# Optimization experiments

Measured on AMD Instinct MI355X. Metric: run time of the kernel, lower is better.

Reference implementation:

```python
import jax, jax.numpy as jnp
import numpy as np

DIM = 768
NUM_HEADS = 12
WIN = (32, 32)  # pretrain window == runtime (H, W)


def _build_rel_pos_idx(wh, ww):
    coords = np.stack(np.meshgrid(np.arange(wh), np.arange(ww), indexing='ij'))  # (2,wh,ww)
    flat = coords.reshape(2, -1)  # (2, N)
    rel = flat[:, :, None] - flat[:, None, :]  # (2, N, N)
    rel = rel.transpose(1, 2, 0).astype(np.int64)  # (N, N, 2)
    rel[:, :, 0] += wh - 1
    rel[:, :, 1] += ww - 1
    rel[:, :, 0] *= 2 * ww - 1
    return rel.sum(-1)  # (N, N) in [0, (2wh-1)(2ww-1))


def setup_inputs() -> dict:
    key = jax.random.key(0)
    ks = jax.random.split(key, 7)
    wh, ww = WIN
    num_rel = (2 * wh - 1) * (2 * ww - 1) + 3  # 3972
    x = jax.random.normal(ks[0], (8, wh, ww, DIM), dtype=jnp.float32)
    qkv_w = jax.random.normal(ks[1], (3 * DIM, DIM), dtype=jnp.float32) * 0.02
    q_bias = jnp.zeros((DIM,), dtype=jnp.float32)
    v_bias = jnp.zeros((DIM,), dtype=jnp.float32)
    rel_bias_table = jax.random.normal(ks[2], (num_rel, NUM_HEADS), dtype=jnp.float32) * 0.02
    proj_w = jax.random.normal(ks[3], (DIM, DIM), dtype=jnp.float32) * 0.02
    proj_b = jnp.zeros((DIM,), dtype=jnp.float32)
    rel_pos_idx = jnp.asarray(_build_rel_pos_idx(wh, ww), dtype=jnp.int32)  # (N, N)
    return {"x": x, "qkv_w": qkv_w, "q_bias": q_bias, "v_bias": v_bias,
            "rel_bias_table": rel_bias_table, "proj_w": proj_w, "proj_b": proj_b,
            "rel_pos_idx": rel_pos_idx}


def reference(x, qkv_w, q_bias, v_bias, rel_bias_table, proj_w, proj_b, rel_pos_idx):
    B, H, W, C = x.shape
    nH = rel_bias_table.shape[-1]
    hd = C // nH
    N = H * W
    scale = hd ** -0.5
    # qkv with (q_bias, 0, v_bias) bias layout as in BEiT
    qkv_bias = jnp.concatenate([q_bias, jnp.zeros_like(v_bias), v_bias])
    qkv = x.reshape(B, N, C) @ qkv_w.T + qkv_bias  # (B, N, 3C)
    qkv = qkv.reshape(B, N, 3, nH, hd).transpose(2, 0, 3, 1, 4)  # (3, B, nH, N, hd)
    q, k, v = qkv[0], qkv[1], qkv[2]
    attn = jnp.einsum('bhnd,bhmd->bhnm', q * scale, k)  # (B, nH, N, N)
    # gathered relative-position bias: table[(N,N)] -> (N, N, nH) -> (nH, N, N)
    bias = rel_bias_table[rel_pos_idx].transpose(2, 0, 1)
    attn = jax.nn.softmax(attn + bias[None], axis=-1)
    out = jnp.einsum('bhnm,bhmd->bhnd', attn, v)  # (B, nH, N, hd)
    out = out.transpose(0, 2, 1, 3).reshape(B, H, W, C)
    return out @ proj_w.T + proj_b
```

## Files before the change

kernel.cpp:

```cpp
#include <hip/hip_runtime.h>
#include <stdint.h>

using u16 = unsigned short;
using u32 = unsigned int;

typedef __bf16 bf16x8 __attribute__((ext_vector_type(8)));
typedef float f32x4 __attribute__((ext_vector_type(4)));

__device__ __forceinline__ u16 f2bf(float f){
  u32 u = __float_as_uint(f);
  return (u16)((u + 0x7FFFu + ((u >> 16) & 1u)) >> 16);
}
__device__ __forceinline__ float bf2f(u16 h){
  return __uint_as_float(((u32)h) << 16);
}
__device__ __forceinline__ void split2(float x, u16& hi, u16& lo){
  hi = f2bf(x);
  lo = f2bf(x - bf2f(hi));
}
template<int SH>
__device__ __forceinline__ int swz(int off){ return off ^ (((off >> SH) & 7) << 4); }

__device__ __forceinline__ void gload16(const u16* g, u16* l){
  __builtin_amdgcn_global_load_lds(
      (const __attribute__((address_space(1))) void*)g,
      (__attribute__((address_space(3))) void*)l, 16, 0, 0);
}

__global__ __launch_bounds__(256) void k_split(const float* __restrict__ src,
                                               u16* __restrict__ hi,
                                               u16* __restrict__ lo)
{
  int i = blockIdx.x * 256 + threadIdx.x;
  float4 v = ((const float4*)src)[i];
  ushort4 h, l;
  split2(v.x, h.x, l.x);
  split2(v.y, h.y, l.y);
  split2(v.z, h.z, l.z);
  split2(v.w, h.w, l.w);
  ((ushort4*)hi)[i] = h;
  ((ushort4*)lo)[i] = l;
}

__global__ __launch_bounds__(256) void k_bias(const int* __restrict__ relidx,
                                              const float* __restrict__ table,
                                              u16* __restrict__ bias)
{
  int q = blockIdx.x;
  int j0 = threadIdx.x * 4;
  int4 idx = *(const int4*)(relidx + q * 1024 + j0);
#pragma unroll
  for (int h = 0; h < 12; ++h){
    ushort4 o;
    o.x = f2bf(table[(size_t)idx.x * 12 + h]);
    o.y = f2bf(table[(size_t)idx.y * 12 + h]);
    o.z = f2bf(table[(size_t)idx.z * 12 + h]);
    o.w = f2bf(table[(size_t)idx.w * 12 + h]);
    *(ushort4*)(bias + ((size_t)h << 20) + q * 1024 + j0) = o;
  }
}

__global__ __launch_bounds__(512) void k_g256(
    const u16* __restrict__ A0, const u16* __restrict__ A1, const u16* __restrict__ A2,
    const u16* __restrict__ B0, const u16* __restrict__ B1, const u16* __restrict__ B2,
    const float* __restrict__ bq, const float* __restrict__ bv,
    u16* __restrict__ QKhi, u16* __restrict__ QKlo,
    u16* __restrict__ Vthi, u16* __restrict__ Vtlo)
{
  extern __shared__ u16 R[];
  const int tid = threadIdx.x;
  const int lane = tid & 63;
  const int wid = tid >> 6;
  const int wm = wid >> 2, wn = wid & 3;
  const int g = lane >> 4, cl = lane & 15;
  const int orig = blockIdx.y * gridDim.x + blockIdx.x;
  const int cpx = (gridDim.x * gridDim.y) >> 3;
  const int wg = (orig & 7) * cpx + (orig >> 3);
  const int bx = wg % gridDim.x, by = wg / gridDim.x;
  const int bm = by << 8, bn = bx << 8;
  const int rlane = lane >> 2;
  const int csrc = (lane & 3) ^ ((lane >> 3) & 3);

  f32x4 acc[8][4];
  f32x4 z4 = {0.f, 0.f, 0.f, 0.f};
#pragma unroll
  for (int i = 0; i < 8; ++i)
#pragma unroll
    for (int j = 0; j < 4; ++j) acc[i][j] = z4;

  auto stageA = [&](int t){
    int tt = (t < 72) ? t : t - 72;
    int ph = (tt >= 48) ? 2 : ((tt >= 24) ? 1 : 0);
    int kin = (tt - ph * 24) * 32;
    const u16* Ap = ph == 0 ? A0 : (ph == 1 ? A1 : A2);
    const int sb = (t & 3) * 16384;
#pragma unroll
    for (int i = 0; i < 2; ++i){
      int rA = (wid * 2 + i) * 16 + rlane;
      gload16(Ap + (size_t)(bm + rA) * 768 + kin + csrc * 8,
              &R[sb + (wid * 2 + i) * 512]);
    }
  };
  auto stageB = [&](int t){
    int tt = (t < 72) ? t : t - 72;
    int ph = (tt >= 48) ? 2 : ((tt >= 24) ? 1 : 0);
    int kin = (tt - ph * 24) * 32;
    const u16* Bp = ph == 0 ? B0 : (ph == 1 ? B1 : B2);
    const int sb = (t & 3) * 16384 + 8192;
#pragma unroll
    for (int i = 0; i < 2; ++i){
      int rB = (wid * 2 + i) * 16 + rlane;
      gload16(Bp + (size_t)(bn + rB) * 768 + kin + csrc * 8,
              &R[sb + (wid * 2 + i) * 512]);
    }
  };
  auto rf = [&](const u16* base, int row) -> bf16x8 {
    return *(const bf16x8*)(base + row * 32 + ((g ^ ((cl >> 1) & 3)) << 3));
  };

  stageA(0); stageB(0); stageA(1); stageB(1); stageA(2); stageB(2);

  for (int t = 0; t < 72; ++t){
    asm volatile("s_waitcnt vmcnt(8)" ::: "memory");
    __builtin_amdgcn_s_barrier();
    __builtin_amdgcn_sched_barrier(0);
    const u16* Ab = &R[(t & 3) * 16384];
    const u16* Bb = Ab + 8192;
    stageA(t + 3);
    bf16x8 bfv[4], af[4];
#pragma unroll
    for (int nf = 0; nf < 4; ++nf) bfv[nf] = rf(Bb, wn * 64 + nf * 16 + cl);
#pragma unroll
    for (int mf = 0; mf < 4; ++mf) af[mf] = rf(Ab, wm * 128 + mf * 16 + cl);
    asm volatile("s_waitcnt lgkmcnt(0)" ::: "memory");
    __builtin_amdgcn_sched_barrier(0);
    __builtin_amdgcn_s_setprio(1);
#pragma unroll
    for (int mf = 0; mf < 4; ++mf)
#pragma unroll
      for (int nf = 0; nf < 4; ++nf)
        acc[mf][nf] = __builtin_amdgcn_mfma_f32_16x16x32_bf16(af[mf], bfv[nf], acc[mf][nf], 0, 0, 0);
    __builtin_amdgcn_s_setprio(0);
    __builtin_amdgcn_s_barrier();
    __builtin_amdgcn_sched_barrier(0);
    stageB(t + 3);
#pragma unroll
    for (int mf = 0; mf < 4; ++mf) af[mf] = rf(Ab, wm * 128 + (mf + 4) * 16 + cl);
    asm volatile("s_waitcnt lgkmcnt(0)" ::: "memory");
    __builtin_amdgcn_sched_barrier(0);
    __builtin_amdgcn_s_setprio(1);
#pragma unroll
    for (int mf = 0; mf < 4; ++mf)
#pragma unroll
      for (int nf = 0; nf < 4; ++nf)
        acc[mf + 4][nf] = __builtin_amdgcn_mfma_f32_16x16x32_bf16(af[mf], bfv[nf], acc[mf + 4][nf], 0, 0, 0);
    __builtin_amdgcn_s_setprio(0);
  }

  const int bb = bm >> 10;
  const int tokb = bm & 1023;
  u16* Hs = R;
  u16* Ls = R + 8192;

  if (bx < 6){
    const bool isQ = (bx < 3);
#pragma unroll
    for (int c = 0; c < 8; ++c){
      __syncthreads();
      if (wm == (c >> 2)){
#pragma unroll
        for (int mi = 0; mi < 2; ++mi){
          const int mf = (c & 3) * 2 + mi;
#pragma unroll
          for (int nf = 0; nf < 4; ++nf){
            int col = wn * 64 + nf * 16 + cl;
            float bqv = isQ ? bq[bn + col] : 0.f;
#pragma unroll
            for (int r = 0; r < 4; ++r){
              float v = acc[mf][nf][r];
              if (isQ) v = (v + bqv) * 0.125f;
              u16 hi, lo; split2(v, hi, lo);
              int idx = (mi * 16 + g * 4 + r) * 256 + col;
              Hs[idx] = hi;
              Ls[idx] = lo;
            }
          }
        }
      }
      __syncthreads();
#pragma unroll
      for (int i = 0; i < 2; ++i){
        int s = tid + i * 512;
        int rr = s >> 5, seg = s & 31;
        size_t gb = (size_t)(bm + c * 32 + rr) * 1536 + bn + seg * 8;
        *(float4*)(QKhi + gb) = *(const float4*)(Hs + rr * 256 + seg * 8);
        *(float4*)(QKlo + gb) = *(const float4*)(Ls + rr * 256 + seg * 8);
      }
    }
  } else {
    const int ccolbase = bn - 1536;
#pragma unroll
    for (int c = 0; c < 8; ++c){
      __syncthreads();
      if (wn == (c >> 1)){
#pragma unroll
        for (int nf2 = 0; nf2 < 2; ++nf2){
          const int nf = (c & 1) * 2 + nf2;
          int cc = nf2 * 16 + cl;
          float bvv = bv[ccolbase + c * 32 + cc];
#pragma unroll
          for (int mf = 0; mf < 8; ++mf){
            ushort4 h4, l4;
            u16 hh_, ll_;
            split2(acc[mf][nf][0] + bvv, hh_, ll_); h4.x = hh_; l4.x = ll_;
            split2(acc[mf][nf][1] + bvv, hh_, ll_); h4.y = hh_; l4.y = ll_;
            split2(acc[mf][nf][2] + bvv, hh_, ll_); h4.z = hh_; l4.z = ll_;
            split2(acc[mf][nf][3] + bvv, hh_, ll_); h4.w = hh_; l4.w = ll_;
            int m0 = wm * 128 + mf * 16 + g * 4;
            int off = cc * 512 + m0 * 2;
            *(ushort4*)((char*)Hs + swz<9>(off)) = h4;
            *(ushort4*)((char*)Ls + swz<9>(off)) = l4;
          }
        }
      }
      __syncthreads();
#pragma unroll
      for (int i = 0; i < 2; ++i){
        int s = tid + i * 512;
        int drr = s >> 5, seg = s & 31;
        int off = drr * 512 + seg * 16;
        int ccol = ccolbase + c * 32 + drr;
        int hh = ccol >> 6, d = ccol & 63;
        size_t gb = ((size_t)(bb * 12 + hh) * 64 + d) * 1024 + tokb + seg * 8;
        *(float4*)(Vthi + gb) = *(const float4*)((char*)Hs + swz<9>(off));
        *(float4*)(Vtlo + gb) = *(const float4*)((char*)Ls + swz<9>(off));
      }
    }
  }
}

__global__ __launch_bounds__(256) void k_proj(
    const u16* __restrict__ A0, const u16* __restrict__ A1, const u16* __restrict__ A2,
    const u16* __restrict__ B0, const u16* __restrict__ B1, const u16* __restrict__ B2,
    const float* __restrict__ pb,
    float* __restrict__ Cout)
{
  __shared__ __align__(16) u16 As[4][128 * 32];
  __shared__ __align__(16) u16 Bs[4][128 * 32];
  const int tid = threadIdx.x;
  const int lane = tid & 63;
  const int wid = tid >> 6;
  const int wr = wid >> 1, wc = wid & 1;
  const int g = lane >> 4, cl = lane & 15;
  const int orig = blockIdx.y * gridDim.x + blockIdx.x;
  const int cpx = (gridDim.x * gridDim.y) >> 3;
  const int wg = (orig & 7) * cpx + (orig >> 3);
  const int bx = wg % gridDim.x, by = wg / gridDim.x;
  const int bm = by << 7, bn = bx << 7;
  const int srow = lane >> 2;
  const int sseg = ((lane & 3) ^ ((lane >> 3) & 3)) * 8;
  const int gph  = (g ^ ((cl >> 1) & 3)) * 8;

  f32x4 acc[4][4];
  f32x4 z4 = {0.f, 0.f, 0.f, 0.f};
#pragma unroll
  for (int i = 0; i < 4; ++i)
#pragma unroll
    for (int j = 0; j < 4; ++j) acc[i][j] = z4;

  auto stage = [&](int t){
    int tt = (t < 72) ? t : t - 72;
    int ph = (tt >= 48) ? 2 : ((tt >= 24) ? 1 : 0);
    int kin = (tt - ph * 24) * 32;
    const u16* Ap = ph == 0 ? A0 : (ph == 1 ? A1 : A2);
    const u16* Bp = ph == 0 ? B0 : (ph == 1 ? B1 : B2);
    const int slot = t & 3;
#pragma unroll
    for (int c = 0; c < 2; ++c){
      int chunk = wid * 2 + c;
      int row = chunk * 16 + srow;
      gload16(Ap + (size_t)(bm + row) * 768 + kin + sseg, &As[slot][chunk * 512]);
      gload16(Bp + (size_t)(bn + row) * 768 + kin + sseg, &Bs[slot][chunk * 512]);
    }
  };

  stage(0); stage(1); stage(2);
  for (int t = 0; t < 72; ++t){
    asm volatile("s_waitcnt vmcnt(8)" ::: "memory");
    __builtin_amdgcn_s_barrier();
    __builtin_amdgcn_sched_barrier(0);
    stage(t + 3);
    const int slot = t & 3;
    bf16x8 af[4], bfv[4];
#pragma unroll
    for (int mf = 0; mf < 4; ++mf)
      af[mf] = *(const bf16x8*)(&As[slot][(wr * 64 + mf * 16 + cl) * 32 + gph]);
#pragma unroll
    for (int nf = 0; nf < 4; ++nf)
      bfv[nf] = *(const bf16x8*)(&Bs[slot][(wc * 64 + nf * 16 + cl) * 32 + gph]);
    asm volatile("s_waitcnt lgkmcnt(0)" ::: "memory");
    __builtin_amdgcn_sched_barrier(0);
    __builtin_amdgcn_s_setprio(1);
#pragma unroll
    for (int mf = 0; mf < 4; ++mf)
#pragma unroll
      for (int nf = 0; nf < 4; ++nf)
        acc[mf][nf] = __builtin_amdgcn_mfma_f32_16x16x32_bf16(af[mf], bfv[nf], acc[mf][nf], 0, 0, 0);
    __builtin_amdgcn_s_setprio(0);
  }

  __syncthreads();
#pragma unroll
  for (int mf = 0; mf < 4; ++mf)
#pragma unroll
    for (int nf = 0; nf < 4; ++nf)
#pragma unroll
      for (int r = 0; r < 4; ++r){
        int m = bm + wr * 64 + mf * 16 + g * 4 + r;
        int n = bn + wc * 64 + nf * 16 + cl;
        Cout[(size_t)m * 768 + n] = acc[mf][nf][r] + pb[n];
      }
}

__global__ __launch_bounds__(256) void k_attn(
    const u16* __restrict__ QKhi, const u16* __restrict__ QKlo,
    const u16* __restrict__ Vthi, const u16* __restrict__ Vtlo,
    const u16* __restrict__ bias,
    u16* __restrict__ Ohi, u16* __restrict__ Olo)
{
  __shared__ __align__(16) u16 lds[36864];
  const int KH0 = 0, KL0 = 8192, VH0 = 16384, VL0 = 24576, PS = 32768;

  const int tid = threadIdx.x;
  const int lane = tid & 63;
  const int w = tid >> 6;
  const int g = lane >> 4, cl = lane & 15;
  const int qt = blockIdx.x;
  const int b  = blockIdx.y;
  const int h  = blockIdx.z;
  const size_t rowbase = (size_t)b * 1024;
  const size_t bhv = (size_t)(b * 12 + h) * (1024 * 64);
  const u16* bias_w = bias + ((size_t)h << 20) + (size_t)(qt * 64 + w * 16) * 1024;

  const int dr = lane >> 3, dc = lane & 7;
  const int csrc = dc ^ dr;
  const size_t kbase = (rowbase + w * 16 + dr) * 1536 + 768 + (size_t)h * 64 + csrc * 8;
  const size_t vbase = bhv + (size_t)(w * 16 + dr) * 1024 + csrc * 8;

  auto stage = [&](int buf, int jt){
#pragma unroll
    for (int i = 0; i < 2; ++i){
      int r0 = (w * 16 + i * 8) * 64;
      size_t ko = kbase + (size_t)(jt * 64 + i * 8) * 1536;
      size_t vo = vbase + (size_t)i * 8 * 1024 + jt * 64;
      gload16(QKhi + ko, &lds[KH0 + buf * 4096 + r0]);
      gload16(QKlo + ko, &lds[KL0 + buf * 4096 + r0]);
      gload16(Vthi + vo, &lds[VH0 + buf * 4096 + r0]);
      gload16(Vtlo + vo, &lds[VL0 + buf * 4096 + r0]);
    }
  };
  auto tread = [&](int base, int r, int cb) -> bf16x8 {
    int byte = r * 128 + ((cb ^ (r & 7)) << 4);
    return *(const bf16x8*)((const char*)&lds[base] + byte);
  };

  bf16x8 aq[4];
  {
    const u16* qh = QKhi + (rowbase + qt * 64 + w * 16 + cl) * 1536 + h * 64;
    const u16* ql = QKlo + (rowbase + qt * 64 + w * 16 + cl) * 1536 + h * 64;
    aq[0] = *(const bf16x8*)(qh + g * 8);
    aq[1] = *(const bf16x8*)(qh + 32 + g * 8);
    aq[2] = *(const bf16x8*)(ql + g * 8);
    aq[3] = *(const bf16x8*)(ql + 32 + g * 8);
  }

  f32x4 o[4];
  float m_run[4], l_run[4];
  f32x4 z4 = {0.f, 0.f, 0.f, 0.f};
#pragma unroll
  for (int nd = 0; nd < 4; ++nd) o[nd] = z4;
#pragma unroll
  for (int r = 0; r < 4; ++r){ m_run[r] = -1e30f; l_run[r] = 0.f; }

  const int AI[6] = {0, 1, 0, 1, 2, 3};
  const int BI[6] = {0, 1, 2, 3, 0, 1};

  stage(0, 0);
  int buf = 0;
  for (int jt = 0; jt < 16; ++jt){
    __syncthreads();
    if (jt + 1 < 16) stage(buf ^ 1, jt + 1);

    f32x4 s[4];
#pragma unroll
    for (int nf = 0; nf < 4; ++nf) s[nf] = z4;
#pragma unroll
    for (int ks = 0; ks < 6; ++ks){
      const int t = BI[ks];
      const int kb = (t >= 2 ? KL0 : KH0) + buf * 4096;
      const int cb = (t & 1) * 4 + g;
      bf16x8 b4[4];
#pragma unroll
      for (int nf = 0; nf < 4; ++nf)
        b4[nf] = tread(kb, nf * 16 + cl, cb);
#pragma unroll
      for (int nf = 0; nf < 4; ++nf)
        s[nf] = __builtin_amdgcn_mfma_f32_16x16x32_bf16(aq[AI[ks]], b4[nf], s[nf], 0, 0, 0);
    }

#pragma unroll
    for (int nf = 0; nf < 4; ++nf){
      int jc = jt * 64 + nf * 16 + cl;
#pragma unroll
      for (int r = 0; r < 4; ++r)
        s[nf][r] += bf2f(bias_w[(size_t)(g * 4 + r) * 1024 + jc]);
    }
#pragma unroll
    for (int r = 0; r < 4; ++r){
      float mx = fmaxf(fmaxf(s[0][r], s[1][r]), fmaxf(s[2][r], s[3][r]));
      mx = fmaxf(mx, __shfl_xor(mx, 1));
      mx = fmaxf(mx, __shfl_xor(mx, 2));
      mx = fmaxf(mx, __shfl_xor(mx, 4));
      mx = fmaxf(mx, __shfl_xor(mx, 8));
      float mn = fmaxf(m_run[r], mx);
      float fs = __expf(m_run[r] - mn);
      m_run[r] = mn;
      float rs = 0.f;
#pragma unroll
      for (int nf = 0; nf < 4; ++nf){
        float p = __expf(s[nf][r] - mn);
        s[nf][r] = p;
        rs += p;
      }
      rs += __shfl_xor(rs, 1);
      rs += __shfl_xor(rs, 2);
      rs += __shfl_xor(rs, 4);
      rs += __shfl_xor(rs, 8);
      l_run[r] = l_run[r] * fs + rs;
#pragma unroll
      for (int nd = 0; nd < 4; ++nd) o[nd][r] *= fs;
    }
#pragma unroll
    for (int nf = 0; nf < 4; ++nf)
#pragma unroll
      for (int r = 0; r < 4; ++r){
        int off = (w * 16 + g * 4 + r) * 128 + (nf * 16 + cl) * 2;
        *(u16*)((char*)&lds[PS] + swz<7>(off)) = f2bf(s[nf][r]);
      }

    bf16x8 pa[2];
    {
      int row = (w * 16 + cl) * 128;
      pa[0] = *(const bf16x8*)((char*)&lds[PS] + swz<7>(row + (g * 8) * 2));
      pa[1] = *(const bf16x8*)((char*)&lds[PS] + swz<7>(row + (32 + g * 8) * 2));
    }
#pragma unroll
    for (int ks = 0; ks < 4; ++ks){
      const int vb = (ks < 2 ? VH0 : VL0) + buf * 4096;
      const int cb = (ks & 1) * 4 + g;
      bf16x8 b4[4];
#pragma unroll
      for (int nd = 0; nd < 4; ++nd)
        b4[nd] = tread(vb, nd * 16 + cl, cb);
#pragma unroll
      for (int nd = 0; nd < 4; ++nd)
        o[nd] = __builtin_amdgcn_mfma_f32_16x16x32_bf16(pa[ks & 1], b4[nd], o[nd], 0, 0, 0);
    }
    buf ^= 1;
  }

  __syncthreads();
#pragma unroll
  for (int r = 0; r < 4; ++r){
    float inv = 1.f / l_run[r];
    int row = w * 16 + g * 4 + r;
#pragma unroll
    for (int nd = 0; nd < 4; ++nd){
      u16 hi, lo; split2(o[nd][r] * inv, hi, lo);
      int off = row * 128 + (nd * 16 + cl) * 2;
      *(u16*)((char*)&lds[PS]  + swz<7>(off)) = hi;
      *(u16*)((char*)&lds[KH0] + swz<7>(off)) = lo;
    }
  }
  __syncthreads();
#pragma unroll
  for (int i = 0; i < 2; ++i){
    int s = tid + i * 256;
    int qr = s >> 3;
    int seg = s & 7;
    int off = qr * 128 + seg * 16;
    size_t gb = ((size_t)b * 1024 + qt * 64 + qr) * 768 + h * 64 + seg * 8;
    *(float4*)(Ohi + gb) = *(const float4*)((char*)&lds[PS]  + swz<7>(off));
    *(float4*)(Olo + gb) = *(const float4*)((char*)&lds[KH0] + swz<7>(off));
  }
}

extern "C" void kernel_launch(void* const* d_in, const int* in_sizes, int n_in,
                              void* d_out, int out_size, void* d_ws, size_t ws_size,
                              hipStream_t stream)
{
  const float* x      = (const float*)d_in[0];
  const float* qkv_w  = (const float*)d_in[1];
  const float* q_bias = (const float*)d_in[2];
  const float* v_bias = (const float*)d_in[3];
  const float* table  = (const float*)d_in[4];
  const float* proj_w = (const float*)d_in[5];
  const float* proj_b = (const float*)d_in[6];
  const int*   relidx = (const int*)d_in[7];
  float* out = (float*)d_out;

  char* ws = (char*)d_ws;
  size_t off = 0;
  auto alloc = [&](size_t nelem) -> u16* {
    u16* p = (u16*)(ws + off);
    off += (nelem * 2 + 255) & ~(size_t)255;
    return p;
  };
  u16* Xhi  = alloc((size_t)8192 * 768);
  u16* Xlo  = alloc((size_t)8192 * 768);
  u16* Whi  = alloc((size_t)2304 * 768);
  u16* Wlo  = alloc((size_t)2304 * 768);
  u16* PWhi = alloc((size_t)768 * 768);
  u16* PWlo = alloc((size_t)768 * 768);
  u16* QKhi = alloc((size_t)8192 * 1536);
  u16* QKlo = alloc((size_t)8192 * 1536);
  u16* Vthi = alloc((size_t)8 * 12 * 64 * 1024);
  u16* Vtlo = alloc((size_t)8 * 12 * 64 * 1024);
  u16* Bias = alloc((size_t)12 * 1024 * 1024);
  u16* Ohi = Xhi;
  u16* Olo = Xlo;

  k_split<<<6144, 256, 0, stream>>>(x, Xhi, Xlo);
  k_split<<<1728, 256, 0, stream>>>(qkv_w, Whi, Wlo);
  k_split<<<576,  256, 0, stream>>>(proj_w, PWhi, PWlo);
  k_bias<<<1024, 256, 0, stream>>>(relidx, table, Bias);

  k_g256<<<dim3(9, 32), 512, 131072, stream>>>(
      Xhi, Xhi, Xlo, Whi, Wlo, Whi,
      q_bias, v_bias,
      QKhi, QKlo, Vthi, Vtlo);

  k_attn<<<dim3(16, 8, 12), 256, 0, stream>>>(
      QKhi, QKlo, Vthi, Vtlo, Bias, Ohi, Olo);

  k_proj<<<dim3(6, 64), 256, 0, stream>>>(
      Ohi, Ohi, Olo, PWhi, PWlo, PWhi,
      proj_b, out);
}
```

Baseline: 418.1 us.

## Shrink QKV GEMM tile to 128x256 with 256 threads and triple-buffered LDS

The QKV projection GEMM moves from 256x256 tiles with 512 threads and a 4-stage 128KB dynamic LDS ring to 128x256 tiles with 256 threads and a 3-stage 72KB static LDS ring. The grid doubles to 576 blocks, which gives better CU coverage and may allow more than one block per CU. The epilogues are rewritten for the new tile shape. In exchange, each block reuses less data per tile and prefetches less deeply, which may expose more memory latency.

```diff
diff --git a/kernel.cpp b/kernel.cpp
--- a/kernel.cpp
+++ b/kernel.cpp
@@ -60,26 +60,26 @@
   }
 }
 
-__global__ __launch_bounds__(512) void k_g256(
+__global__ __launch_bounds__(256) void k_g256(
     const u16* __restrict__ A0, const u16* __restrict__ A1, const u16* __restrict__ A2,
     const u16* __restrict__ B0, const u16* __restrict__ B1, const u16* __restrict__ B2,
     const float* __restrict__ bq, const float* __restrict__ bv,
     u16* __restrict__ QKhi, u16* __restrict__ QKlo,
     u16* __restrict__ Vthi, u16* __restrict__ Vtlo)
 {
-  extern __shared__ u16 R[];
+  __shared__ __align__(16) u16 R[36864];
   const int tid = threadIdx.x;
   const int lane = tid & 63;
   const int wid = tid >> 6;
-  const int wm = wid >> 2, wn = wid & 3;
   const int g = lane >> 4, cl = lane & 15;
   const int orig = blockIdx.y * gridDim.x + blockIdx.x;
   const int cpx = (gridDim.x * gridDim.y) >> 3;
   const int wg = (orig & 7) * cpx + (orig >> 3);
   const int bx = wg % gridDim.x, by = wg / gridDim.x;
-  const int bm = by << 8, bn = bx << 8;
+  const int bm = by << 7, bn = bx << 8;
   const int rlane = lane >> 2;
   const int csrc = (lane & 3) ^ ((lane >> 3) & 3);
+  const int gph  = (g ^ ((cl >> 1) & 3)) << 3;
 
   f32x4 acc[8][4];
   f32x4 z4 = {0.f, 0.f, 0.f, 0.f};
@@ -93,12 +93,11 @@
     int ph = (tt >= 48) ? 2 : ((tt >= 24) ? 1 : 0);
     int kin = (tt - ph * 24) * 32;
     const u16* Ap = ph == 0 ? A0 : (ph == 1 ? A1 : A2);
-    const int sb = (t & 3) * 16384;
+    u16* S = &R[(t % 3) * 12288];
 #pragma unroll
     for (int i = 0; i < 2; ++i){
-      int rA = (wid * 2 + i) * 16 + rlane;
-      gload16(Ap + (size_t)(bm + rA) * 768 + kin + csrc * 8,
-              &R[sb + (wid * 2 + i) * 512]);
+      int row = wid * 32 + i * 16;
+      gload16(Ap + (size_t)(bm + row + rlane) * 768 + kin + csrc * 8, S + row * 32);
     }
   };
   auto stageB = [&](int t){
@@ -106,32 +105,30 @@
     int ph = (tt >= 48) ? 2 : ((tt >= 24) ? 1 : 0);
     int kin = (tt - ph * 24) * 32;
     const u16* Bp = ph == 0 ? B0 : (ph == 1 ? B1 : B2);
-    const int sb = (t & 3) * 16384 + 8192;
-#pragma unroll
-    for (int i = 0; i < 2; ++i){
-      int rB = (wid * 2 + i) * 16 + rlane;
-      gload16(Bp + (size_t)(bn + rB) * 768 + kin + csrc * 8,
-              &R[sb + (wid * 2 + i) * 512]);
+    u16* S = &R[(t % 3) * 12288 + 4096];
+#pragma unroll
+    for (int j = 0; j < 4; ++j){
+      int row = wid * 64 + j * 16;
+      gload16(Bp + (size_t)(bn + row + rlane) * 768 + kin + csrc * 8, S + row * 32);
     }
   };
-  auto rf = [&](const u16* base, int row) -> bf16x8 {
-    return *(const bf16x8*)(base + row * 32 + ((g ^ ((cl >> 1) & 3)) << 3));
-  };
-
-  stageA(0); stageB(0); stageA(1); stageB(1); stageA(2); stageB(2);
+
+  stageA(0); stageB(0); stageA(1); stageB(1);
 
   for (int t = 0; t < 72; ++t){
-    asm volatile("s_waitcnt vmcnt(8)" ::: "memory");
+    asm volatile("s_waitcnt vmcnt(6)" ::: "memory");
     __builtin_amdgcn_s_barrier();
     __builtin_amdgcn_sched_barrier(0);
-    const u16* Ab = &R[(t & 3) * 16384];
-    const u16* Bb = Ab + 8192;
-    stageA(t + 3);
+    const u16* Ab = &R[(t % 3) * 12288];
+    const u16* Bb = Ab + 4096;
+    stageA(t + 2);
     bf16x8 bfv[4], af[4];
 #pragma unroll
-    for (int nf = 0; nf < 4; ++nf) bfv[nf] = rf(Bb, wn * 64 + nf * 16 + cl);
-#pragma unroll
-    for (int mf = 0; mf < 4; ++mf) af[mf] = rf(Ab, wm * 128 + mf * 16 + cl);
+    for (int nf = 0; nf < 4; ++nf)
+      bfv[nf] = *(const bf16x8*)(Bb + (wid * 64 + nf * 16 + cl) * 32 + gph);
+#pragma unroll
+    for (int mf = 0; mf < 4; ++mf)
+      af[mf] = *(const bf16x8*)(Ab + (mf * 16 + cl) * 32 + gph);
     asm volatile("s_waitcnt lgkmcnt(0)" ::: "memory");
     __builtin_amdgcn_sched_barrier(0);
     __builtin_amdgcn_s_setprio(1);
@@ -143,9 +140,10 @@
     __builtin_amdgcn_s_setprio(0);
     __builtin_amdgcn_s_barrier();
     __builtin_amdgcn_sched_barrier(0);
-    stageB(t + 3);
-#pragma unroll
-    for (int mf = 0; mf < 4; ++mf) af[mf] = rf(Ab, wm * 128 + (mf + 4) * 16 + cl);
+    stageB(t + 2);
+#pragma unroll
+    for (int mf = 0; mf < 4; ++mf)
+      af[mf] = *(const bf16x8*)(Ab + ((mf + 4) * 16 + cl) * 32 + gph);
     asm volatile("s_waitcnt lgkmcnt(0)" ::: "memory");
     __builtin_amdgcn_sched_barrier(0);
     __builtin_amdgcn_s_setprio(1);
@@ -164,50 +162,49 @@
 
   if (bx < 6){
     const bool isQ = (bx < 3);
+    const int colb = bx << 8;
+#pragma unroll
+    for (int c = 0; c < 4; ++c){
+      __syncthreads();
+#pragma unroll
+      for (int mi = 0; mi < 2; ++mi){
+        const int mf = c * 2 + mi;
+#pragma unroll
+        for (int nf = 0; nf < 4; ++nf){
+          int col = wid * 64 + nf * 16 + cl;
+          float bqv = isQ ? bq[colb + col] : 0.f;
+#pragma unroll
+          for (int r = 0; r < 4; ++r){
+            float v = acc[mf][nf][r];
+            if (isQ) v = (v + bqv) * 0.125f;
+            u16 hi, lo; split2(v, hi, lo);
+            int idx = (mi * 16 + g * 4 + r) * 256 + col;
+            Hs[idx] = hi;
+            Ls[idx] = lo;
+          }
+        }
+      }
+      __syncthreads();
+#pragma unroll
+      for (int i = 0; i < 4; ++i){
+        int s = tid + i * 256;
+        int rr = s >> 5, seg = s & 31;
+        size_t gb = (size_t)(bm + c * 32 + rr) * 1536 + colb + seg * 8;
+        *(float4*)(QKhi + gb) = *(const float4*)(Hs + rr * 256 + seg * 8);
+        *(float4*)(QKlo + gb) = *(const float4*)(Ls + rr * 256 + seg * 8);
+      }
+    }
+  } else {
+    const int vb0 = (bx - 6) << 8;
 #pragma unroll
     for (int c = 0; c < 8; ++c){
       __syncthreads();
-      if (wm == (c >> 2)){
-#pragma unroll
-        for (int mi = 0; mi < 2; ++mi){
-          const int mf = (c & 3) * 2 + mi;
-#pragma unroll
-          for (int nf = 0; nf < 4; ++nf){
-            int col = wn * 64 + nf * 16 + cl;
-            float bqv = isQ ? bq[bn + col] : 0.f;
-#pragma unroll
-            for (int r = 0; r < 4; ++r){
-              float v = acc[mf][nf][r];
-              if (isQ) v = (v + bqv) * 0.125f;
-              u16 hi, lo; split2(v, hi, lo);
-              int idx = (mi * 16 + g * 4 + r) * 256 + col;
-              Hs[idx] = hi;
-              Ls[idx] = lo;
-            }
-          }
-        }
-      }
-      __syncthreads();
-#pragma unroll
-      for (int i = 0; i < 2; ++i){
-        int s = tid + i * 512;
-        int rr = s >> 5, seg = s & 31;
-        size_t gb = (size_t)(bm + c * 32 + rr) * 1536 + bn + seg * 8;
-        *(float4*)(QKhi + gb) = *(const float4*)(Hs + rr * 256 + seg * 8);
-        *(float4*)(QKlo + gb) = *(const float4*)(Ls + rr * 256 + seg * 8);
-      }
-    }
-  } else {
-    const int ccolbase = bn - 1536;
-#pragma unroll
-    for (int c = 0; c < 8; ++c){
-      __syncthreads();
-      if (wn == (c >> 1)){
+      if (wid == (c >> 1)){
 #pragma unroll
         for (int nf2 = 0; nf2 < 2; ++nf2){
           const int nf = (c & 1) * 2 + nf2;
           int cc = nf2 * 16 + cl;
-          float bvv = bv[ccolbase + c * 32 + cc];
+          float bvv = bv[vb0 + c * 32 + cc];
 #pragma unroll
           for (int mf = 0; mf < 8; ++mf){
             ushort4 h4, l4;
@@ -216,24 +213,25 @@
             split2(acc[mf][nf][1] + bvv, hh_, ll_); h4.y = hh_; l4.y = ll_;
             split2(acc[mf][nf][2] + bvv, hh_, ll_); h4.z = hh_; l4.z = ll_;
             split2(acc[mf][nf][3] + bvv, hh_, ll_); h4.w = hh_; l4.w = ll_;
-            int m0 = wm * 128 + mf * 16 + g * 4;
-            int off = cc * 512 + m0 * 2;
-            *(ushort4*)((char*)Hs + swz<9>(off)) = h4;
-            *(ushort4*)((char*)Ls + swz<9>(off)) = l4;
+            int m0 = mf * 16 + g * 4;
+            int off = cc * 256 + m0 * 2;
+            *(ushort4*)((char*)Hs + swz<8>(off)) = h4;
+            *(ushort4*)((char*)Ls + swz<8>(off)) = l4;
           }
         }
       }
       __syncthreads();
 #pragma unroll
       for (int i = 0; i < 2; ++i){
-        int s = tid + i * 512;
-        int drr = s >> 5, seg = s & 31;
-        int off = drr * 512 + seg * 16;
-        int ccol = ccolbase + c * 32 + drr;
+        int s = tid + i * 256;
+        int drr = s >> 4;
+        int ms = (s & 15) * 8;
+        int off = drr * 256 + ms * 2;
+        int ccol = vb0 + c * 32 + drr;
         int hh = ccol >> 6, d = ccol & 63;
-        size_t gb = ((size_t)(bb * 12 + hh) * 64 + d) * 1024 + tokb + seg * 8;
-        *(float4*)(Vthi + gb) = *(const float4*)((char*)Hs + swz<9>(off));
-        *(float4*)(Vtlo + gb) = *(const float4*)((char*)Ls + swz<9>(off));
+        size_t gb = ((size_t)(bb * 12 + hh) * 64 + d) * 1024 + tokb + ms;
+        *(float4*)(Vthi + gb) = *(const float4*)((char*)Hs + swz<8>(off));
+        *(float4*)(Vtlo + gb) = *(const float4*)((char*)Ls + swz<8>(off));
       }
     }
   }
@@ -535,7 +533,7 @@
   k_split<<<576,  256, 0, stream>>>(proj_w, PWhi, PWlo);
   k_bias<<<1024, 256, 0, stream>>>(relidx, table, Bias);
 
-  k_g256<<<dim3(9, 32), 512, 131072, stream>>>(
+  k_g256<<<dim3(9, 64), 256, 0, stream>>>(
       Xhi, Xhi, Xlo, Whi, Wlo, Whi,
       q_bias, v_bias,
       QKhi, QKlo, Vthi, Vtlo);
```

New measurement: 462.1 us. 10.5% more time.
